# Kernel optimization log

Hardware: AMD Instinct MI355X
Metric: run time of the kernel (lower is better)

Reference implementation:

```python
import jax, jax.numpy as jnp
import numpy as np

CHUNK = 1024
ROPE_BASE = 10000.0


def _rope_cos_sin(positions, dim, dtype):
    # positions: (nc, C) absolute positions; returns cos/sin of shape (nc, C, dim)
    inv_freq = 1.0 / (ROPE_BASE ** (jnp.arange(0, dim, 2, dtype=jnp.float32) / dim))
    ang = positions.astype(jnp.float32)[..., None] * inv_freq  # (nc, C, dim/2)
    ang = jnp.concatenate([ang, ang], axis=-1)  # rotate-half layout
    return jnp.cos(ang).astype(dtype), jnp.sin(ang).astype(dtype)


def _rotate_half(x):
    x1, x2 = jnp.split(x, 2, axis=-1)
    return jnp.concatenate([-x2, x1], axis=-1)


def setup_inputs() -> dict:
    key = jax.random.key(0)
    kq, kk, kv = jax.random.split(key, 3)
    B, L, H, Dh, Dv = 2, 8192, 16, 64, 64
    return {
        "q": jax.random.normal(kq, (B, L, H, Dh), dtype=jnp.float32),
        "k": jax.random.normal(kk, (B, L, H, Dh), dtype=jnp.float32),
        "v": jax.random.normal(kv, (B, L, H, Dv), dtype=jnp.float32),
        "start_index": 0,
    }


def reference(q, k, v, start_index):
    # Block-diagonal chunked causal attention with inline RoPE, scale = 1.0.
    B, L, H, Dh = q.shape
    Dv = v.shape[-1]
    C = CHUNK
    nc = L // C  # L chosen divisible by chunk_size (pad path is a no-op)

    qc = q.reshape(B, nc, C, H, Dh)
    kc = k.reshape(B, nc, C, H, Dh)
    vc = v.reshape(B, nc, C, H, Dv)

    # Absolute positions per chunk: start_index + chunk_offset + intra-chunk pos
    pos = start_index + jnp.arange(nc)[:, None] * C + jnp.arange(C)[None, :]  # (nc, C)
    cos, sin = _rope_cos_sin(pos, Dh, q.dtype)  # (nc, C, Dh)
    cos = cos[None, :, :, None, :]  # (1, nc, C, 1, Dh)
    sin = sin[None, :, :, None, :]

    q_rot = qc * cos + _rotate_half(qc) * sin
    k_rot = kc * cos + _rotate_half(kc) * sin

    # fp32 scores, NO temperature scaling (scale = 1.0)
    scores = jnp.einsum(
        "bnqhd,bnkhd->bnhqk",
        q_rot.astype(jnp.float32),
        k_rot.astype(jnp.float32),
    )
    causal = jnp.tril(jnp.ones((C, C), dtype=jnp.bool_))
    scores = jnp.where(causal, scores, jnp.finfo(jnp.float32).min)
    attn = jax.nn.softmax(scores, axis=-1)

    out = jnp.einsum("bnhqk,bnkhd->bnqhd", attn, vc.astype(jnp.float32))
    return out.astype(q.dtype).reshape(B, L, H, Dv)
```

## Files before the change

kernel.cpp:

```cpp
#include <hip/hip_runtime.h>
#include <math.h>

typedef _Float16 half8 __attribute__((ext_vector_type(8)));
typedef _Float16 half4 __attribute__((ext_vector_type(4)));
typedef float    floatx4 __attribute__((ext_vector_type(4)));

#define B_   2
#define L_   8192
#define H_   16
#define D_   64
#define C_   1024
#define NC_  8
#define HD_  1024
#define KSTR 72
#define VSTR 40
#define PSTR 40
#define LOG2B 0.41524101186098314f

__device__ __forceinline__ float rormax16(float v) {
    int x;
    x = __builtin_amdgcn_mov_dpp(__float_as_int(v), 0x121, 0xf, 0xf, true); v = fmaxf(v, __int_as_float(x));
    x = __builtin_amdgcn_mov_dpp(__float_as_int(v), 0x122, 0xf, 0xf, true); v = fmaxf(v, __int_as_float(x));
    x = __builtin_amdgcn_mov_dpp(__float_as_int(v), 0x124, 0xf, 0xf, true); v = fmaxf(v, __int_as_float(x));
    x = __builtin_amdgcn_mov_dpp(__float_as_int(v), 0x128, 0xf, 0xf, true); v = fmaxf(v, __int_as_float(x));
    return v;
}

__global__ __launch_bounds__(256, 2)
void attn_v3(const float* __restrict__ qg, const float* __restrict__ kg,
             const float* __restrict__ vg, const int* __restrict__ sidx,
             float* __restrict__ outg)
{
    __shared__ __align__(16) _Float16 Kl[32 * KSTR];
    __shared__ __align__(16) _Float16 Vt[64 * VSTR];
    __shared__ __align__(16) _Float16 Pl[4][16 * PSTR];

    const int t  = threadIdx.x;
    const int w  = t >> 6;
    const int lg = (t >> 4) & 3;
    const int ln = t & 15;

    const int bid = blockIdx.x;
    const int j  = bid & 3;
    const int h  = (bid >> 2) & 15;
    const int n  = (bid >> 6) & 7;
    const int b  = bid >> 9;

    const int p0   = sidx[0] + n * C_;
    const int qoff = j * 64 + w * 16;

    const long bhbase = ((long)b * L_ + (long)n * C_) * HD_ + (long)h * D_;
    const float* kbase = kg + bhbase;
    const float* vbase = vg + bhbase;

    half8 aq[4][2];
    const int d0 = lg * 8;
    #pragma unroll
    for (int s = 0; s < 4; ++s) {
        const int qr = s * 256 + qoff + ln;
        const float* qp = qg + bhbase + (long)qr * HD_;
        float4 f0 = *(const float4*)(qp + d0);
        float4 f1 = *(const float4*)(qp + d0 + 4);
        float4 g0 = *(const float4*)(qp + d0 + 32);
        float4 g1 = *(const float4*)(qp + d0 + 36);
        float x[8] = {f0.x,f0.y,f0.z,f0.w,f1.x,f1.y,f1.z,f1.w};
        float y[8] = {g0.x,g0.y,g0.z,g0.w,g1.x,g1.y,g1.z,g1.w};
        const float pos = (float)(p0 + qr);
        #pragma unroll
        for (int jj = 0; jj < 8; ++jj) {
            float invf = exp2f(-(float)(d0 + jj) * LOG2B);
            float sn, cs; __sincosf(pos * invf, &sn, &cs);
            aq[s][0][jj] = (_Float16)(x[jj] * cs - y[jj] * sn);
            aq[s][1][jj] = (_Float16)(y[jj] * cs + x[jj] * sn);
        }
    }

    floatx4 O[4][4];
    floatx4 Ol[4];
    float   mr[4][4];
    #pragma unroll
    for (int s = 0; s < 4; ++s) {
        Ol[s] = (floatx4){0.f,0.f,0.f,0.f};
        #pragma unroll
        for (int dt = 0; dt < 4; ++dt) O[s][dt] = (floatx4){0.f,0.f,0.f,0.f};
        #pragma unroll
        for (int r = 0; r < 4; ++r) mr[s][r] = -1e30f;
    }
    half8 bones;
    #pragma unroll
    for (int jj = 0; jj < 8; ++jj) bones[jj] = (_Float16)1.0f;

    const int sr = t >> 3;
    const int sc = (t & 7) * 4;
    float sinvk[4];
    #pragma unroll
    for (int i = 0; i < 4; ++i) sinvk[i] = exp2f(-(float)(sc + i) * LOG2B);
    const int vc = t & 31;
    const int vr = (t >> 5) * 4;

    const int NKT = ((831 + j * 64) >> 5) + 1;
    int nkt_s[4];
    #pragma unroll
    for (int s = 0; s < 4; ++s) nkt_s[s] = ((s * 256 + qoff + 15) >> 5) + 1;

    float4 kp0, kp1; float2 vp0, vp1, vp2, vp3;
    {
        const float* kp = kbase + (long)sr * HD_ + sc;
        kp0 = *(const float4*)kp; kp1 = *(const float4*)(kp + 32);
        const float* vp = vbase + (long)vr * HD_ + 2 * vc;
        vp0 = *(const float2*)vp;           vp1 = *(const float2*)(vp + HD_);
        vp2 = *(const float2*)(vp + 2*HD_); vp3 = *(const float2*)(vp + 3*HD_);
    }

    for (int kt = 0; kt < NKT; ++kt) {
        const int kb0 = kt * 32;
        __syncthreads();
        {
            const float pos = (float)(p0 + kb0 + sr);
            float ka[4] = {kp0.x,kp0.y,kp0.z,kp0.w};
            float kc[4] = {kp1.x,kp1.y,kp1.z,kp1.w};
            half4 o0, o1;
            #pragma unroll
            for (int i = 0; i < 4; ++i) {
                float sn, cs; __sincosf(pos * sinvk[i], &sn, &cs);
                o0[i] = (_Float16)(ka[i] * cs - kc[i] * sn);
                o1[i] = (_Float16)(kc[i] * cs + ka[i] * sn);
            }
            *(half4*)(&Kl[sr * KSTR + sc])      = o0;
            *(half4*)(&Kl[sr * KSTR + sc + 32]) = o1;
            half4 va, vb;
            va[0] = (_Float16)vp0.x; va[1] = (_Float16)vp1.x; va[2] = (_Float16)vp2.x; va[3] = (_Float16)vp3.x;
            vb[0] = (_Float16)vp0.y; vb[1] = (_Float16)vp1.y; vb[2] = (_Float16)vp2.y; vb[3] = (_Float16)vp3.y;
            *(half4*)(&Vt[(2 * vc)     * VSTR + vr]) = va;
            *(half4*)(&Vt[(2 * vc + 1) * VSTR + vr]) = vb;
        }
        if (kt + 1 < NKT) {
            const int kb1 = kb0 + 32;
            const float* kp = kbase + (long)(kb1 + sr) * HD_ + sc;
            kp0 = *(const float4*)kp; kp1 = *(const float4*)(kp + 32);
            const float* vp = vbase + (long)(kb1 + vr) * HD_ + 2 * vc;
            vp0 = *(const float2*)vp;           vp1 = *(const float2*)(vp + HD_);
            vp2 = *(const float2*)(vp + 2*HD_); vp3 = *(const float2*)(vp + 3*HD_);
        }
        __syncthreads();

        half8 bk0[2], bk1[2], bv[4];
        #pragma unroll
        for (int ct = 0; ct < 2; ++ct) {
            const _Float16* kr = &Kl[(ct * 16 + ln) * KSTR + lg * 8];
            bk0[ct] = *(const half8*)kr;
            bk1[ct] = *(const half8*)(kr + 32);
        }
        #pragma unroll
        for (int dt = 0; dt < 4; ++dt)
            bv[dt] = *(const half8*)(&Vt[(dt * 16 + ln) * VSTR + lg * 8]);

        #pragma unroll
        for (int s = 0; s < 4; ++s) {
            if (kt >= nkt_s[s]) continue;
            const int qs = s * 256 + qoff;

            floatx4 sacc[2];
            #pragma unroll
            for (int ct = 0; ct < 2; ++ct) {
                floatx4 acc = (floatx4){0.f,0.f,0.f,0.f};
                acc = __builtin_amdgcn_mfma_f32_16x16x32_f16(aq[s][0], bk0[ct], acc, 0, 0, 0);
                acc = __builtin_amdgcn_mfma_f32_16x16x32_f16(aq[s][1], bk1[ct], acc, 0, 0, 0);
                sacc[ct] = acc;
            }
            if (kb0 + 31 > qs) {
                #pragma unroll
                for (int ct = 0; ct < 2; ++ct) {
                    const int kkc = kb0 + ct * 16 + ln;
                    #pragma unroll
                    for (int r = 0; r < 4; ++r)
                        if (kkc > qs + lg * 4 + r) sacc[ct][r] = -1e30f;
                }
            }
            float alpha[4];
            #pragma unroll
            for (int r = 0; r < 4; ++r) {
                float tm   = rormax16(fmaxf(sacc[0][r], sacc[1][r]));
                float mnew = fmaxf(mr[s][r], tm);
                alpha[r]   = __expf(mr[s][r] - mnew);
                mr[s][r]   = mnew;
            }
            #pragma unroll
            for (int r = 0; r < 4; ++r) {
                Ol[s][r] *= alpha[r];
                #pragma unroll
                for (int dt = 0; dt < 4; ++dt) O[s][dt][r] *= alpha[r];
            }
            #pragma unroll
            for (int r = 0; r < 4; ++r) {
                float pa = __expf(sacc[0][r] - mr[s][r]);
                float pb = __expf(sacc[1][r] - mr[s][r]);
                const int qloc = lg * 4 + r;
                Pl[w][qloc * PSTR + ln]      = (_Float16)pa;
                Pl[w][qloc * PSTR + 16 + ln] = (_Float16)pb;
            }
            half8 ap = *(const half8*)(&Pl[w][ln * PSTR + lg * 8]);
            #pragma unroll
            for (int dt = 0; dt < 4; ++dt)
                O[s][dt] = __builtin_amdgcn_mfma_f32_16x16x32_f16(ap, bv[dt], O[s][dt], 0, 0, 0);
            Ol[s] = __builtin_amdgcn_mfma_f32_16x16x32_f16(ap, bones, Ol[s], 0, 0, 0);
        }
    }

    #pragma unroll
    for (int s = 0; s < 4; ++s) {
        const int qs = s * 256 + qoff;
        float inv[4];
        #pragma unroll
        for (int r = 0; r < 4; ++r) inv[r] = 1.0f / Ol[s][r];
        #pragma unroll
        for (int dt = 0; dt < 4; ++dt) {
            #pragma unroll
            for (int r = 0; r < 4; ++r) {
                const int qr = qs + lg * 4 + r;
                outg[bhbase + (long)qr * HD_ + dt * 16 + ln] = O[s][dt][r] * inv[r];
            }
        }
    }
}

extern "C" void kernel_launch(void* const* d_in, const int* in_sizes, int n_in,
                              void* d_out, int out_size, void* d_ws, size_t ws_size,
                              hipStream_t stream) {
    const float* q    = (const float*)d_in[0];
    const float* k    = (const float*)d_in[1];
    const float* v    = (const float*)d_in[2];
    const int*   sidx = (const int*)d_in[3];
    float*       out  = (float*)d_out;

    dim3 grid(B_ * NC_ * H_ * 4);
    dim3 block(256);
    attn_v3<<<grid, block, 0, stream>>>(q, k, v, sidx, out);
}
```

Baseline: 285.4 us.

## Use exp2 softmax with lazy rescale, transposed LDS P reads, higher occupancy

Pre-scales Q by log2(e) so the softmax can use the hardware exp2 and packed fp16 conversion. The running-max rescale of the accumulators now runs only when some row's max grows by more than a threshold. P is staged in a transposed LDS layout and read back with ds_read_b64_tr_b16 instead of scalar stores and a strided read. Launch bounds rise to 4 blocks per SM, and blocks are reordered so the four query slices of a head are spread apart. The lazy rescale loosens the numerical bound on fp16 P values, and higher occupancy may cause register spills.

```diff
diff --git a/kernel.cpp b/kernel.cpp
--- a/kernel.cpp
+++ b/kernel.cpp
@@ -1,8 +1,9 @@
 #include <hip/hip_runtime.h>
 #include <math.h>
 
-typedef _Float16 half8 __attribute__((ext_vector_type(8)));
-typedef _Float16 half4 __attribute__((ext_vector_type(4)));
+typedef _Float16 half8  __attribute__((ext_vector_type(8)));
+typedef _Float16 half4  __attribute__((ext_vector_type(4)));
+typedef __fp16   f16x2  __attribute__((ext_vector_type(2)));
 typedef float    floatx4 __attribute__((ext_vector_type(4)));
 
 #define B_   2
@@ -14,8 +15,22 @@
 #define HD_  1024
 #define KSTR 72
 #define VSTR 40
-#define PSTR 40
 #define LOG2B 0.41524101186098314f
+#define LOG2E 1.4426950408889634f
+#define DTHR  8.0f
+
+__device__ __forceinline__ float fast_exp2(float x) {
+#if __has_builtin(__builtin_amdgcn_exp2f)
+    return __builtin_amdgcn_exp2f(x);
+#else
+    return exp2f(x);
+#endif
+}
+
+__device__ __forceinline__ unsigned pk16(float a, float b) {
+    f16x2 r = __builtin_amdgcn_cvt_pkrtz(a, b);
+    return __builtin_bit_cast(unsigned, r);
+}
 
 __device__ __forceinline__ float rormax16(float v) {
     int x;
@@ -26,14 +41,14 @@
     return v;
 }
 
-__global__ __launch_bounds__(256, 2)
-void attn_v3(const float* __restrict__ qg, const float* __restrict__ kg,
+__global__ __launch_bounds__(256, 4)
+void attn_v4(const float* __restrict__ qg, const float* __restrict__ kg,
              const float* __restrict__ vg, const int* __restrict__ sidx,
              float* __restrict__ outg)
 {
     __shared__ __align__(16) _Float16 Kl[32 * KSTR];
     __shared__ __align__(16) _Float16 Vt[64 * VSTR];
-    __shared__ __align__(16) _Float16 Pl[4][16 * PSTR];
+    __shared__ __align__(16) _Float16 Pt[4][32 * 16];
 
     const int t  = threadIdx.x;
     const int w  = t >> 6;
@@ -41,10 +56,11 @@
     const int ln = t & 15;
 
     const int bid = blockIdx.x;
-    const int j  = bid & 3;
-    const int h  = (bid >> 2) & 15;
-    const int n  = (bid >> 6) & 7;
-    const int b  = bid >> 9;
+    const int j   = bid >> 8;
+    const int grp = bid & 255;
+    const int h   = grp & 15;
+    const int n   = (grp >> 4) & 7;
+    const int b   = grp >> 7;
 
     const int p0   = sidx[0] + n * C_;
     const int qoff = j * 64 + w * 16;
@@ -68,10 +84,10 @@
         const float pos = (float)(p0 + qr);
         #pragma unroll
         for (int jj = 0; jj < 8; ++jj) {
-            float invf = exp2f(-(float)(d0 + jj) * LOG2B);
+            float invf = fast_exp2(-(float)(d0 + jj) * LOG2B);
             float sn, cs; __sincosf(pos * invf, &sn, &cs);
-            aq[s][0][jj] = (_Float16)(x[jj] * cs - y[jj] * sn);
-            aq[s][1][jj] = (_Float16)(y[jj] * cs + x[jj] * sn);
+            aq[s][0][jj] = (_Float16)((x[jj] * cs - y[jj] * sn) * LOG2E);
+            aq[s][1][jj] = (_Float16)((y[jj] * cs + x[jj] * sn) * LOG2E);
         }
     }
 
@@ -94,7 +110,7 @@
     const int sc = (t & 7) * 4;
     float sinvk[4];
     #pragma unroll
-    for (int i = 0; i < 4; ++i) sinvk[i] = exp2f(-(float)(sc + i) * LOG2B);
+    for (int i = 0; i < 4; ++i) sinvk[i] = fast_exp2(-(float)(sc + i) * LOG2B);
     const int vc = t & 31;
     const int vr = (t >> 5) * 4;
 
@@ -102,6 +118,9 @@
     int nkt_s[4];
     #pragma unroll
     for (int s = 0; s < 4; ++s) nkt_s[s] = ((s * 256 + qoff + 15) >> 5) + 1;
+
+    const unsigned trad = (unsigned)(unsigned long long)(uintptr_t)(&Pt[w][0])
+                        + 8u * (unsigned)ln + 256u * (unsigned)lg;
 
     float4 kp0, kp1; float2 vp0, vp1, vp2, vp3;
     {
@@ -177,29 +196,42 @@
                         if (kkc > qs + lg * 4 + r) sacc[ct][r] = -1e30f;
                 }
             }
-            float alpha[4];
+
+            float tm[4];
+            int grow = 0;
             #pragma unroll
             for (int r = 0; r < 4; ++r) {
-                float tm   = rormax16(fmaxf(sacc[0][r], sacc[1][r]));
-                float mnew = fmaxf(mr[s][r], tm);
-                alpha[r]   = __expf(mr[s][r] - mnew);
-                mr[s][r]   = mnew;
-            }
-            #pragma unroll
-            for (int r = 0; r < 4; ++r) {
-                Ol[s][r] *= alpha[r];
+                tm[r] = rormax16(fmaxf(sacc[0][r], sacc[1][r]));
+                grow |= (tm[r] > mr[s][r] + DTHR) ? 1 : 0;
+            }
+            if (__any(grow)) {
                 #pragma unroll
-                for (int dt = 0; dt < 4; ++dt) O[s][dt][r] *= alpha[r];
-            }
-            #pragma unroll
-            for (int r = 0; r < 4; ++r) {
-                float pa = __expf(sacc[0][r] - mr[s][r]);
-                float pb = __expf(sacc[1][r] - mr[s][r]);
-                const int qloc = lg * 4 + r;
-                Pl[w][qloc * PSTR + ln]      = (_Float16)pa;
-                Pl[w][qloc * PSTR + 16 + ln] = (_Float16)pb;
-            }
-            half8 ap = *(const half8*)(&Pl[w][ln * PSTR + lg * 8]);
+                for (int r = 0; r < 4; ++r) {
+                    float mnew  = fmaxf(mr[s][r], tm[r]);
+                    float alpha = fast_exp2(mr[s][r] - mnew);
+                    mr[s][r] = mnew;
+                    Ol[s][r] *= alpha;
+                    #pragma unroll
+                    for (int dt = 0; dt < 4; ++dt) O[s][dt][r] *= alpha;
+                }
+            }
+
+            uint2 wa, wb;
+            wa.x = pk16(fast_exp2(sacc[0][0] - mr[s][0]), fast_exp2(sacc[0][1] - mr[s][1]));
+            wa.y = pk16(fast_exp2(sacc[0][2] - mr[s][2]), fast_exp2(sacc[0][3] - mr[s][3]));
+            wb.x = pk16(fast_exp2(sacc[1][0] - mr[s][0]), fast_exp2(sacc[1][1] - mr[s][1]));
+            wb.y = pk16(fast_exp2(sacc[1][2] - mr[s][2]), fast_exp2(sacc[1][3] - mr[s][3]));
+            *(uint2*)(&Pt[w][ ln       * 16 + lg * 4]) = wa;
+            *(uint2*)(&Pt[w][(16 + ln) * 16 + lg * 4]) = wb;
+            asm volatile("s_waitcnt lgkmcnt(0)" ::: "memory");
+            half4 tlo, thi;
+            asm volatile("ds_read_b64_tr_b16 %0, %2\n\t"
+                         "ds_read_b64_tr_b16 %1, %2 offset:128"
+                         : "=&v"(tlo), "=&v"(thi) : "v"(trad));
+            asm volatile("s_waitcnt lgkmcnt(0)" ::: "memory");
+            __builtin_amdgcn_sched_barrier(0);
+            half8 ap = __builtin_shufflevector(tlo, thi, 0, 1, 2, 3, 4, 5, 6, 7);
+
             #pragma unroll
             for (int dt = 0; dt < 4; ++dt)
                 O[s][dt] = __builtin_amdgcn_mfma_f32_16x16x32_f16(ap, bv[dt], O[s][dt], 0, 0, 0);
@@ -235,5 +267,5 @@
 
     dim3 grid(B_ * NC_ * H_ * 4);
     dim3 block(256);
-    attn_v3<<<grid, block, 0, stream>>>(q, k, v, sidx, out);
-}
+    attn_v4<<<grid, block, 0, stream>>>(q, k, v, sidx, out);
+}
```

New measurement: 809.7 us. 184% more time.
